# Optimization experiments

Measured on AMD Instinct MI355X. Metric: run time of the kernel, lower is better.

## Reference

```python
import jax, jax.numpy as jnp
import numpy as np

N = 32000      # total nodes (16 graphs x 2000 nodes)
B = 16         # batch of graphs
NPG = N // B   # nodes per graph
K = 1600       # assign_dim (total clusters)
KPG = K // B   # clusters per graph
D = 128        # input_dim == output_feat_dim
E = 512000     # edges (avg degree 16), block-diagonal across graphs


def setup_inputs() -> dict:
    key = jax.random.key(0)
    ks = jax.random.split(key, 12)
    # block-structured edge list: each edge stays within its graph
    epg = E // B
    gid = jnp.repeat(jnp.arange(B, dtype=jnp.int32), epg) * NPG
    src = gid + jax.random.randint(ks[0], (E,), 0, NPG, dtype=jnp.int32)
    dst = gid + jax.random.randint(ks[1], (E,), 0, NPG, dtype=jnp.int32)
    h = jax.random.normal(ks[2], (N, D), dtype=jnp.float32)
    s = 0.05
    return {
        'h': h, 'src': src, 'dst': dst,
        'W1f': jax.random.normal(ks[3], (D, D), jnp.float32) * s,
        'b1f': jnp.zeros((D,), jnp.float32),
        'W2f': jax.random.normal(ks[4], (D, D), jnp.float32) * s,
        'b2f': jnp.zeros((D,), jnp.float32),
        'W1p': jax.random.normal(ks[5], (D, K), jnp.float32) * s,
        'b1p': jnp.zeros((K,), jnp.float32),
        'W2p': jax.random.normal(ks[6], (K, K), jnp.float32) * s,
        'b2p': jnp.zeros((K,), jnp.float32),
    }


def _gin(h, src, dst, W1, b1, W2, b2):
    # mean-aggregate neighbor features, then 2-layer MLP (histocartography GINLayer)
    deg = jax.ops.segment_sum(jnp.ones((src.shape[0],), h.dtype), dst, num_segments=N)
    agg = jax.ops.segment_sum(h[src], dst, num_segments=N)
    agg = agg / jnp.maximum(deg, 1.0)[:, None]
    x = h + agg
    x = jax.nn.relu(x @ W1 + b1)
    x = jax.nn.relu(x @ W2 + b2)
    return x


def _forward(h, src, dst, W1f, b1f, W2f, b2f, W1p, b1p, W2p, b2p):
    feat = _gin(h, src, dst, W1f, b1f, W2f, b2f)            # [N, D]
    assign = _gin(h, src, dst, W1p, b1p, W2p, b2p)          # [N, K]
    # block-diagonal mask: node of graph b can only assign to clusters of graph b
    node_gid = jnp.arange(N, dtype=jnp.int32) // NPG
    col_gid = jnp.arange(K, dtype=jnp.int32) // KPG
    mask = (node_gid[:, None] == col_gid[None, :]).astype(assign.dtype)  # [N, K]
    # masked_softmax(memory_efficient=False): softmax(x*mask)*mask, renormalized
    p = jax.nn.softmax(assign * mask, axis=-1) * mask
    assign = p / (jnp.sum(p, axis=-1, keepdims=True) + 1e-13)
    h_pool = assign.T @ feat                                # [K, D]
    # adj @ assign where adj[dst, src] = 1 (sparse-dense mm via scatter)
    tmp = jax.ops.segment_sum(assign[src], dst, num_segments=N)  # [N, K]
    adj_new = assign.T @ tmp                                # [K, K]
    return adj_new, h_pool


def reference(h, src, dst, W1f, b1f, W2f, b2f, W1p, b1p, W2p, b2p):
    return _forward(h, src, dst, W1f, b1f, W2f, b2f, W1p, b1p, W2p, b2p)
```

## Files before the change

### kernel.cpp

```cpp
#include <hip/hip_runtime.h>

#define N_NODES 32000
#define NPG     2000
#define NGRAPH  16
#define K_ASSIGN 1600
#define KPG     100
#define D_FEAT  128
#define N_EDGES 512000

typedef float f32x4 __attribute__((ext_vector_type(4)));
typedef __bf16 bf16x8 __attribute__((ext_vector_type(8)));

union FragU { unsigned u[4]; bf16x8 v; };

__device__ __forceinline__ float frelu(float v) { return fmaxf(v, 0.0f); }

__device__ __forceinline__ unsigned short f2bf(float f) {
  unsigned u = __float_as_uint(f);
  u += 0x7FFFu + ((u >> 16) & 1u);
  return (unsigned short)(u >> 16);
}
__device__ __forceinline__ float bfLO(unsigned v) { return __uint_as_float(v << 16); }
__device__ __forceinline__ float bfHI(unsigned v) { return __uint_as_float(v & 0xFFFF0000u); }

__global__ __launch_bounds__(256) void edge_hist(
    const int* __restrict__ dst, int* __restrict__ cnt) {
  int e = blockIdx.x * 256 + threadIdx.x;
  if (e < N_EDGES) atomicAdd(&cnt[dst[e]], 1);
}

__global__ __launch_bounds__(256) void scan_counts(
    const int* __restrict__ cnt, int* __restrict__ rowstart) {
  __shared__ int sums[256];
  int t = threadIdx.x;
  int base = t * 125;
  int s = 0;
  for (int i = 0; i < 125; i++) s += cnt[base + i];
  sums[t] = s;
  __syncthreads();
  for (int off = 1; off < 256; off <<= 1) {
    int v = (t >= off) ? sums[t - off] : 0;
    __syncthreads();
    sums[t] += v;
    __syncthreads();
  }
  int run = (t == 0) ? 0 : sums[t - 1];
  for (int i = 0; i < 125; i++) {
    rowstart[base + i] = run;
    run += cnt[base + i];
  }
  if (t == 255) rowstart[32000] = run;
}

__global__ __launch_bounds__(256) void edge_fill(
    const int* __restrict__ src, const int* __restrict__ dst,
    const int* __restrict__ rowstart, int* __restrict__ cursor,
    int* __restrict__ bucket) {
  int e = blockIdx.x * 256 + threadIdx.x;
  if (e < N_EDGES) {
    int d = dst[e];
    int pos = atomicAdd(&cursor[d], 1);
    bucket[rowstart[d] + pos] = src[e];
  }
}

__global__ __launch_bounds__(256) void h_to_bf(
    const float* __restrict__ h, unsigned short* __restrict__ hb) {
  int i = blockIdx.x * 256 + threadIdx.x;
  float4 v = ((const float4*)h)[i];
  ushort4 o;
  o.x = f2bf(v.x); o.y = f2bf(v.y); o.z = f2bf(v.z); o.w = f2bf(v.w);
  ((ushort4*)hb)[i] = o;
}

__global__ __launch_bounds__(256) void gin_gather(
    const int* __restrict__ rowstart, const int* __restrict__ bucket,
    const float* __restrict__ h, const unsigned short* __restrict__ h_bf,
    unsigned short* __restrict__ x_bf) {
  int n = blockIdx.x * 4 + (threadIdx.x >> 6);
  int lane = threadIdx.x & 63;
  int rs = rowstart[n], re = rowstart[n + 1];
  const unsigned* hb = (const unsigned*)h_bf;
  float ax = 0.f, ay = 0.f;
  int e = rs;
  for (; e + 4 <= re; e += 4) {
    unsigned v0 = hb[(size_t)bucket[e] * 64 + lane];
    unsigned v1 = hb[(size_t)bucket[e + 1] * 64 + lane];
    unsigned v2 = hb[(size_t)bucket[e + 2] * 64 + lane];
    unsigned v3 = hb[(size_t)bucket[e + 3] * 64 + lane];
    ax += (bfLO(v0) + bfLO(v1)) + (bfLO(v2) + bfLO(v3));
    ay += (bfHI(v0) + bfHI(v1)) + (bfHI(v2) + bfHI(v3));
  }
  for (; e < re; e++) {
    unsigned v = hb[(size_t)bucket[e] * 64 + lane];
    ax += bfLO(v);
    ay += bfHI(v);
  }
  float invd = 1.0f / fmaxf((float)(re - rs), 1.0f);
  float2 hv = ((const float2*)h)[(size_t)n * 64 + lane];
  unsigned o = ((unsigned)f2bf(hv.y + ay * invd) << 16) | f2bf(hv.x + ax * invd);
  ((unsigned*)x_bf)[(size_t)n * 64 + lane] = o;
}

__global__ __launch_bounds__(256) void transpose_all(
    const float* __restrict__ W1f, const float* __restrict__ W2f,
    const float* __restrict__ W1p, const float* __restrict__ W2p,
    unsigned short* __restrict__ o1, unsigned short* __restrict__ o2,
    unsigned short* __restrict__ o3, unsigned short* __restrict__ o4) {
  __shared__ float tile[32][33];
  int b = blockIdx.x;
  const float* in;
  unsigned short* out;
  int R, C, rb;
  if (b < 16)       { in = W1f; out = o1; R = 128;  C = 128;  rb = b; }
  else if (b < 32)  { in = W2f; out = o2; R = 128;  C = 128;  rb = b - 16; }
  else if (b < 232) { in = W1p; out = o3; R = 128;  C = 1600; rb = b - 32; }
  else              { in = W2p; out = o4; R = 1600; C = 1600; rb = b - 232; }
  int ct = C >> 5;
  int bc = rb % ct, br = rb / ct;
  int r0 = br * 32, c0 = bc * 32;
  int t = threadIdx.x;
#pragma unroll
  for (int i = 0; i < 4; i++) {
    int r = (t >> 5) + i * 8, c = t & 31;
    tile[r][c] = in[(size_t)(r0 + r) * C + c0 + c];
  }
  __syncthreads();
#pragma unroll
  for (int i = 0; i < 4; i++) {
    int c = (t >> 5) + i * 8, r = t & 31;
    out[(size_t)(c0 + c) * R + r0 + r] = f2bf(tile[r][c]);
  }
}

#define FF_STR 136
__global__ __launch_bounds__(512) void feat_fused(
    const unsigned short* __restrict__ x_bf,
    const unsigned short* __restrict__ w1t, const float* __restrict__ b1f,
    const unsigned short* __restrict__ w2t, const float* __restrict__ b2f,
    unsigned short* __restrict__ feat_bf) {
  __shared__ __align__(16) unsigned char smem[2 * 34816];
  unsigned short* xa = (unsigned short*)smem;
  unsigned short* ws = (unsigned short*)(smem + 34816);
  int t = threadIdx.x;
  size_t base = (size_t)blockIdx.x * 128;

#pragma unroll
  for (int i = 0; i < 4; i++) {
    int fi = t + 512 * i;
    int r = fi >> 4, u8 = (fi & 15) * 8;
    *(uint4*)&xa[r * FF_STR + u8] = *(const uint4*)(x_bf + (base + r) * 128 + u8);
    *(uint4*)&ws[r * FF_STR + u8] = *(const uint4*)(w1t + (size_t)r * 128 + u8);
  }
  __syncthreads();

  int w = t >> 6, l = t & 63, lr = l & 15, lg = l >> 4;
  int myrow = 16 * w + lr;
  bf16x8 af[4];
#pragma unroll
  for (int kc = 0; kc < 4; kc++)
    af[kc] = *(bf16x8*)&xa[myrow * FF_STR + 32 * kc + 8 * lg];

  f32x4 p[8];
#pragma unroll
  for (int ntk = 0; ntk < 8; ntk++) {
    p[ntk] = (f32x4){0.f, 0.f, 0.f, 0.f};
    int c = 16 * ntk + lr;
#pragma unroll
    for (int kc = 0; kc < 4; kc++) {
      bf16x8 wf = *(bf16x8*)&ws[c * FF_STR + 32 * kc + 8 * lg];
      p[ntk] = __builtin_amdgcn_mfma_f32_16x16x32_bf16(wf, af[kc], p[ntk], 0, 0, 0);
    }
  }
  __syncthreads();

#pragma unroll
  for (int ntk = 0; ntk < 8; ntk++) {
    int kk0 = 16 * ntk + 4 * lg;
    float4 b1 = *(const float4*)(b1f + kk0);
    ushort4 pk;
    pk.x = f2bf(frelu(p[ntk][0] + b1.x));
    pk.y = f2bf(frelu(p[ntk][1] + b1.y));
    pk.z = f2bf(frelu(p[ntk][2] + b1.z));
    pk.w = f2bf(frelu(p[ntk][3] + b1.w));
    *(ushort4*)&xa[myrow * FF_STR + kk0] = pk;
  }
#pragma unroll
  for (int i = 0; i < 4; i++) {
    int fi = t + 512 * i;
    int r = fi >> 4, u8 = (fi & 15) * 8;
    *(uint4*)&ws[r * FF_STR + u8] = *(const uint4*)(w2t + (size_t)r * 128 + u8);
  }
  __syncthreads();

  bf16x8 a2[4];
#pragma unroll
  for (int kc = 0; kc < 4; kc++)
    a2[kc] = *(bf16x8*)&xa[myrow * FF_STR + 32 * kc + 8 * lg];
#pragma unroll
  for (int nt = 0; nt < 8; nt++) {
    f32x4 q = (f32x4){0.f, 0.f, 0.f, 0.f};
    int c = 16 * nt + lr;
#pragma unroll
    for (int kc = 0; kc < 4; kc++) {
      bf16x8 wf = *(bf16x8*)&ws[c * FF_STR + 32 * kc + 8 * lg];
      q = __builtin_amdgcn_mfma_f32_16x16x32_bf16(wf, a2[kc], q, 0, 0, 0);
    }
    int c0 = 16 * nt + 4 * lg;
    float4 b2 = *(const float4*)(b2f + c0);
    ushort4 pk;
    pk.x = f2bf(frelu(q[0] + b2.x));
    pk.y = f2bf(frelu(q[1] + b2.y));
    pk.z = f2bf(frelu(q[2] + b2.z));
    pk.w = f2bf(frelu(q[3] + b2.w));
    *(ushort4*)&feat_bf[(base + myrow) * 128 + c0] = pk;
  }
}

#define FA_WS 136
#define FA_PS 72
#define FA_W1OFF 17408
#define FA_W2BASE 34816
#define FA_W2OFF 16128
__global__ __launch_bounds__(512) void fused_assign_sm(
    const unsigned short* __restrict__ x_bf, const unsigned short* __restrict__ w1t,
    const float* __restrict__ b1p, const unsigned short* __restrict__ w2t,
    const float* __restrict__ b2p, unsigned short* __restrict__ assign_bf) {
  __shared__ __align__(16) unsigned char smem[67072];
  unsigned short* xt = (unsigned short*)smem;

  int t = threadIdx.x;
  int g = blockIdx.x >> 4;
  int row0 = (blockIdx.x & 15) << 7;
  int n0 = g * NPG + row0;

#pragma unroll
  for (int i = 0; i < 4; i++) {
    int fi = t + 512 * i;
    int r = fi >> 4, u8 = (fi & 15) * 8;
    uint4 v = make_uint4(0, 0, 0, 0);
    if (row0 + r < NPG) v = *(const uint4*)(x_bf + (size_t)(n0 + r) * 128 + u8);
    *(uint4*)&xt[r * FA_WS + u8] = v;
  }
  __syncthreads();

  int w = t >> 6, l = t & 63, lr = l & 15, lg = l >> 4;
  int rh = w >> 1, h = w & 1;

  bf16x8 af[2][4];
#pragma unroll
  for (int ct = 0; ct < 2; ct++)
#pragma unroll
    for (int kc = 0; kc < 4; kc++)
      af[ct][kc] =
          *(bf16x8*)&xt[(32 * rh + 16 * ct + lr) * FA_WS + 32 * kc + 8 * lg];
  __syncthreads();

  {
    unsigned short* w1s = (unsigned short*)smem;
    unsigned short* w2s = (unsigned short*)(smem + FA_W2BASE);
#pragma unroll
    for (int i = 0; i < 2; i++) {
      int fi = t + 512 * i;
      int c = fi >> 4, u8 = (fi & 15) * 8;
      *(uint4*)&w1s[c * FA_WS + u8] = *(const uint4*)(w1t + (size_t)c * 128 + u8);
    }
#pragma unroll
    for (int i = 0; i < 2; i++) {
      int fi = t + 512 * i;
      if (fi < 896) {
        int c = fi >> 3, u8 = (fi & 7) * 8;
        uint4 v = make_uint4(0, 0, 0, 0);
        if (c < KPG)
          v = *(const uint4*)(w2t + (size_t)(g * KPG + c) * K_ASSIGN + u8);
        *(uint4*)&w2s[c * FA_PS + u8] = v;
      }
    }
  }
  __syncthreads();

  f32x4 acc[7][2];
#pragma unroll
  for (int i = 0; i < 7; i++) {
    acc[i][0] = (f32x4){0.f, 0.f, 0.f, 0.f};
    acc[i][1] = (f32x4){0.f, 0.f, 0.f, 0.f};
  }

  for (int cch = 0; cch < 25; cch++) {
    int cur = cch & 1;
    int k0 = cch * 64;
    const unsigned short* w1c = (const unsigned short*)(smem + cur * FA_W1OFF);
    const unsigned short* w2c =
        (const unsigned short*)(smem + FA_W2BASE + cur * FA_W2OFF);
    bool pf = (cch < 24);
    uint4 rA[2], rB[2];
    if (pf) {
      int k1 = k0 + 64;
#pragma unroll
      for (int i = 0; i < 2; i++) {
        int fi = t + 512 * i;
        int c = fi >> 4, u8 = (fi & 15) * 8;
        rA[i] = *(const uint4*)(w1t + (size_t)(k1 + c) * 128 + u8);
      }
#pragma unroll
      for (int i = 0; i < 2; i++) {
        int fi = t + 512 * i;
        rB[i] = make_uint4(0, 0, 0, 0);
        if (fi < 896) {
          int c = fi >> 3, u8 = (fi & 7) * 8;
          if (c < KPG)
            rB[i] = *(const uint4*)(w2t + (size_t)(g * KPG + c) * K_ASSIGN +
                                    k1 + u8);
        }
      }
    }

    f32x4 p[2][2];
#pragma unroll
    for (int nt2 = 0; nt2 < 2; nt2++) {
      p[nt2][0] = (f32x4){0.f, 0.f, 0.f, 0.f};
      p[nt2][1] = (f32x4){0.f, 0.f, 0.f, 0.f};
      int nt = 2 * h + nt2;
#pragma unroll
      for (int kc = 0; kc < 4; kc++) {
        bf16x8 wf = *(bf16x8*)&w1c[(16 * nt + lr) * FA_WS + 32 * kc + 8 * lg];
        p[nt2][0] = __builtin_amdgcn_mfma_f32_16x16x32_bf16(wf, af[0][kc],
                                                            p[nt2][0], 0, 0, 0);
        p[nt2][1] = __builtin_amdgcn_mfma_f32_16x16x32_bf16(wf, af[1][kc],
                                                            p[nt2][1], 0, 0, 0);
      }
    }
    unsigned q[2][2][2];
#pragma unroll
    for (int nt2 = 0; nt2 < 2; nt2++) {
      int kkb = k0 + 16 * (2 * h + nt2) + 4 * lg;
      float4 b1 = *(const float4*)(b1p + kkb);
#pragma unroll
      for (int ct = 0; ct < 2; ct++) {
        float r0 = frelu(p[nt2][ct][0] + b1.x);
        float r1 = frelu(p[nt2][ct][1] + b1.y);
        float r2 = frelu(p[nt2][ct][2] + b1.z);
        float r3 = frelu(p[nt2][ct][3] + b1.w);
        q[nt2][ct][0] = ((unsigned)f2bf(r1) << 16) | f2bf(r0);
        q[nt2][ct][1] = ((unsigned)f2bf(r3) << 16) | f2bf(r2);
      }
    }
    int sA = lr + 32 * (lg & 1);
    int sB = sA + 16;
    bool hi = (lg >= 2);
    FragU pa[2];
#pragma unroll
    for (int ct = 0; ct < 2; ct++) {
      unsigned a0 = (unsigned)__shfl((int)q[0][ct][0], sA, 64);
      unsigned b0 = (unsigned)__shfl((int)q[1][ct][0], sA, 64);
      unsigned a1 = (unsigned)__shfl((int)q[0][ct][1], sA, 64);
      unsigned b1u = (unsigned)__shfl((int)q[1][ct][1], sA, 64);
      unsigned a2 = (unsigned)__shfl((int)q[0][ct][0], sB, 64);
      unsigned b2u = (unsigned)__shfl((int)q[1][ct][0], sB, 64);
      unsigned a3 = (unsigned)__shfl((int)q[0][ct][1], sB, 64);
      unsigned b3u = (unsigned)__shfl((int)q[1][ct][1], sB, 64);
      pa[ct].u[0] = hi ? b0 : a0;
      pa[ct].u[1] = hi ? b1u : a1;
      pa[ct].u[2] = hi ? b2u : a2;
      pa[ct].u[3] = hi ? b3u : a3;
    }
#pragma unroll
    for (int ct2 = 0; ct2 < 7; ct2++) {
      bf16x8 wv = *(bf16x8*)&w2c[(16 * ct2 + lr) * FA_PS + 32 * h + 8 * lg];
      acc[ct2][0] = __builtin_amdgcn_mfma_f32_16x16x32_bf16(wv, pa[0].v,
                                                            acc[ct2][0], 0, 0, 0);
      acc[ct2][1] = __builtin_amdgcn_mfma_f32_16x16x32_bf16(wv, pa[1].v,
                                                            acc[ct2][1], 0, 0, 0);
    }
    if (pf) {
      unsigned short* w1n = (unsigned short*)(smem + (cur ^ 1) * FA_W1OFF);
      unsigned short* w2n =
          (unsigned short*)(smem + FA_W2BASE + (cur ^ 1) * FA_W2OFF);
#pragma unroll
      for (int i = 0; i < 2; i++) {
        int fi = t + 512 * i;
        int c = fi >> 4, u8 = (fi & 15) * 8;
        *(uint4*)&w1n[c * FA_WS + u8] = rA[i];
      }
#pragma unroll
      for (int i = 0; i < 2; i++) {
        int fi = t + 512 * i;
        if (fi < 896) {
          int c = fi >> 3, u8 = (fi & 7) * 8;
          *(uint4*)&w2n[c * FA_PS + u8] = rB[i];
        }
      }
    }
    __syncthreads();
  }

  float* red = (float*)smem;
  if (h == 1) {
#pragma unroll
    for (int ct2 = 0; ct2 < 7; ct2++)
#pragma unroll
      for (int ct = 0; ct < 2; ct++)
        *(f32x4*)&red[((rh * 14 + ct2 * 2 + ct) * 64 + l) * 4] = acc[ct2][ct];
  }
  __syncthreads();
  if (h == 0) {
#pragma unroll
    for (int ct2 = 0; ct2 < 7; ct2++)
#pragma unroll
      for (int ct = 0; ct < 2; ct++)
        acc[ct2][ct] += *(f32x4*)&red[((rh * 14 + ct2 * 2 + ct) * 64 + l) * 4];

#pragma unroll
    for (int ct = 0; ct < 2; ct++) {
      int xrow = row0 + 32 * rh + 16 * ct + lr;
      float v[7][4];
      float m = 0.0f;
#pragma unroll
      for (int ct2 = 0; ct2 < 7; ct2++) {
        int col0 = 16 * ct2 + 4 * lg;
        if (col0 < KPG) {
          float4 b2 = *(const float4*)(b2p + g * KPG + col0);
          v[ct2][0] = frelu(acc[ct2][ct][0] + b2.x);
          v[ct2][1] = frelu(acc[ct2][ct][1] + b2.y);
          v[ct2][2] = frelu(acc[ct2][ct][2] + b2.z);
          v[ct2][3] = frelu(acc[ct2][ct][3] + b2.w);
          m = fmaxf(m, fmaxf(fmaxf(v[ct2][0], v[ct2][1]),
                             fmaxf(v[ct2][2], v[ct2][3])));
        }
      }
      m = fmaxf(m, __shfl_xor(m, 16, 64));
      m = fmaxf(m, __shfl_xor(m, 32, 64));
      float s = 0.0f;
#pragma unroll
      for (int ct2 = 0; ct2 < 7; ct2++) {
        int col0 = 16 * ct2 + 4 * lg;
        if (col0 < KPG) {
          v[ct2][0] = expf(v[ct2][0] - m);
          v[ct2][1] = expf(v[ct2][1] - m);
          v[ct2][2] = expf(v[ct2][2] - m);
          v[ct2][3] = expf(v[ct2][3] - m);
          s += (v[ct2][0] + v[ct2][1]) + (v[ct2][2] + v[ct2][3]);
        }
      }
      s += __shfl_xor(s, 16, 64);
      s += __shfl_xor(s, 32, 64);
      float denom = s + (float)(K_ASSIGN - KPG) * expf(-m);
      float scale = 1.0f / (s + 1e-13f * denom);
      if (xrow < NPG) {
#pragma unroll
        for (int ct2 = 0; ct2 < 7; ct2++) {
          int col0 = 16 * ct2 + 4 * lg;
          if (col0 < KPG) {
            ushort4 pk;
            pk.x = f2bf(v[ct2][0] * scale);
            pk.y = f2bf(v[ct2][1] * scale);
            pk.z = f2bf(v[ct2][2] * scale);
            pk.w = f2bf(v[ct2][3] * scale);
            *(ushort4*)(assign_bf + ((size_t)g * NPG + xrow) * KPG + col0) = pk;
          }
        }
      }
    }
  }
}

__global__ __launch_bounds__(256) void tmp_gather(
    const int* __restrict__ rowstart, const int* __restrict__ bucket,
    const unsigned short* __restrict__ assign_bf, unsigned short* __restrict__ tmp_bf) {
  int n = blockIdx.x * 4 + (threadIdx.x >> 6);
  int lane = threadIdx.x & 63;
  if (lane >= 50) return;
  int rs = rowstart[n], re = rowstart[n + 1];
  const unsigned* ab = (const unsigned*)assign_bf;
  float ax = 0.f, ay = 0.f;
  int e = rs;
  for (; e + 4 <= re; e += 4) {
    unsigned v0 = ab[(size_t)bucket[e] * 50 + lane];
    unsigned v1 = ab[(size_t)bucket[e + 1] * 50 + lane];
    unsigned v2 = ab[(size_t)bucket[e + 2] * 50 + lane];
    unsigned v3 = ab[(size_t)bucket[e + 3] * 50 + lane];
    ax += (bfLO(v0) + bfLO(v1)) + (bfLO(v2) + bfLO(v3));
    ay += (bfHI(v0) + bfHI(v1)) + (bfHI(v2) + bfHI(v3));
  }
  for (; e < re; e++) {
    unsigned v = ab[(size_t)bucket[e] * 50 + lane];
    ax += bfLO(v);
    ay += bfHI(v);
  }
  unsigned o = ((unsigned)f2bf(ay) << 16) | f2bf(ax);
  ((unsigned*)tmp_bf)[(size_t)n * 50 + lane] = o;
}

#define PA_STR 72
#define PA_CH 16
#define PA_CHN 128
__global__ __launch_bounds__(256) void pool_adj_mfma(
    const unsigned short* __restrict__ assign_bf,
    const unsigned short* __restrict__ feat_bf,
    const unsigned short* __restrict__ tmp_bf,
    float* __restrict__ out_adj, float* __restrict__ out_hpool) {
  __shared__ __align__(16) unsigned short as[112 * PA_STR];
  __shared__ __align__(16) unsigned short bs[128 * PA_STR];
  bool is_pool = blockIdx.x < NGRAPH * PA_CH;
  int bb = is_pool ? blockIdx.x : blockIdx.x - NGRAPH * PA_CH;
  int g = bb >> 4, ch = bb & 15;
  int nbase = ch * PA_CHN;
  int lim = NPG - nbase;
  if (lim > PA_CHN) lim = PA_CHN;
  int t = threadIdx.x;
  int w = t >> 6, l = t & 63, lr = l & 15, lg = l >> 4;
  const unsigned* au = (const unsigned*)assign_bf;
  const unsigned* fu = (const unsigned*)feat_bf;
  const unsigned* tu = (const unsigned*)tmp_bf;

  for (int i = t; i < 12 * PA_STR; i += 256) as[100 * PA_STR + i] = 0;
  for (int i = t; i < 28 * PA_STR; i += 256) bs[100 * PA_STR + i] = 0;

  f32x4 acc[7][2];
#pragma unroll
  for (int i = 0; i < 7; i++) {
    acc[i][0] = (f32x4){0.f, 0.f, 0.f, 0.f};
    acc[i][1] = (f32x4){0.f, 0.f, 0.f, 0.f};
  }

  for (int kt = 0; kt < 2; kt++) {
    int nt0 = kt * 64;
    __syncthreads();
#pragma unroll
    for (int i = 0; i < 13; i++) {
      int idx = t + 256 * i;
      if (idx < 3200) {
        int r = idx / 50, cu = idx % 50;
        int nl = nt0 + r;
        unsigned v = 0;
        if (nl < lim) v = au[(size_t)(g * NPG + nbase + nl) * 50 + cu];
        as[(2 * cu) * PA_STR + r] = (unsigned short)(v & 0xFFFFu);
        as[(2 * cu + 1) * PA_STR + r] = (unsigned short)(v >> 16);
      }
    }
    if (is_pool) {
#pragma unroll
      for (int i = 0; i < 16; i++) {
        int idx = t + 256 * i;
        int r = idx >> 6, cu = idx & 63;
        int nl = nt0 + r;
        unsigned v = 0;
        if (nl < lim) v = fu[(size_t)(g * NPG + nbase + nl) * 64 + cu];
        bs[(2 * cu) * PA_STR + r] = (unsigned short)(v & 0xFFFFu);
        bs[(2 * cu + 1) * PA_STR + r] = (unsigned short)(v >> 16);
      }
    } else {
#pragma unroll
      for (int i = 0; i < 13; i++) {
        int idx = t + 256 * i;
        if (idx < 3200) {
          int r = idx / 50, cu = idx % 50;
          int nl = nt0 + r;
          unsigned v = 0;
          if (nl < lim) v = tu[(size_t)(g * NPG + nbase + nl) * 50 + cu];
          bs[(2 * cu) * PA_STR + r] = (unsigned short)(v & 0xFFFFu);
          bs[(2 * cu + 1) * PA_STR + r] = (unsigned short)(v >> 16);
        }
      }
    }
    __syncthreads();
#pragma unroll
    for (int kc = 0; kc < 2; kc++) {
      bf16x8 afr[7];
#pragma unroll
      for (int mt = 0; mt < 7; mt++)
        afr[mt] = *(bf16x8*)&as[(16 * mt + lr) * PA_STR + 32 * kc + 8 * lg];
#pragma unroll
      for (int nt2 = 0; nt2 < 2; nt2++) {
        int nt = 2 * w + nt2;
        bf16x8 bfr = *(bf16x8*)&bs[(16 * nt + lr) * PA_STR + 32 * kc + 8 * lg];
#pragma unroll
        for (int mt = 0; mt < 7; mt++)
          acc[mt][nt2] =
              __builtin_amdgcn_mfma_f32_16x16x32_bf16(afr[mt], bfr, acc[mt][nt2], 0, 0, 0);
      }
    }
  }

  if (is_pool) {
#pragma unroll
    for (int mt = 0; mt < 7; mt++)
#pragma unroll
      for (int nt2 = 0; nt2 < 2; nt2++) {
        int nt = 2 * w + nt2;
#pragma unroll
        for (int r = 0; r < 4; r++) {
          int m = 16 * mt + 4 * lg + r;
          if (m < KPG)
            atomicAdd(out_hpool + ((size_t)g * KPG + m) * 128 + 16 * nt + lr,
                      acc[mt][nt2][r]);
        }
      }
  } else {
#pragma unroll
    for (int mt = 0; mt < 7; mt++)
#pragma unroll
      for (int nt2 = 0; nt2 < 2; nt2++) {
        int nt = 2 * w + nt2;
        if (nt < 7) {
          int k2 = 16 * nt + lr;
          if (k2 < KPG) {
#pragma unroll
            for (int r = 0; r < 4; r++) {
              int m = 16 * mt + 4 * lg + r;
              if (m < KPG)
                atomicAdd(out_adj + ((size_t)g * KPG + m) * K_ASSIGN + g * KPG + k2,
                          acc[mt][nt2][r]);
            }
          }
        }
      }
  }
}

extern "C" void kernel_launch(void* const* d_in, const int* in_sizes, int n_in,
                              void* d_out, int out_size, void* d_ws,
                              size_t ws_size, hipStream_t stream) {
  (void)in_sizes; (void)n_in; (void)ws_size;
  const float* h   = (const float*)d_in[0];
  const int*   src = (const int*)d_in[1];
  const int*   dst = (const int*)d_in[2];
  const float* W1f = (const float*)d_in[3];
  const float* b1f = (const float*)d_in[4];
  const float* W2f = (const float*)d_in[5];
  const float* b2f = (const float*)d_in[6];
  const float* W1p = (const float*)d_in[7];
  const float* b1p = (const float*)d_in[8];
  const float* W2p = (const float*)d_in[9];
  const float* b2p = (const float*)d_in[10];

  float* out_adj   = (float*)d_out;
  float* out_hpool = out_adj + (size_t)K_ASSIGN * K_ASSIGN;

  char* ws = (char*)d_ws;
  int* deg_cnt  = (int*)(ws + 0);
  int* rowstart = (int*)(ws + 128000);
  int* cursor   = (int*)(ws + 256032);
  int* bucket   = (int*)(ws + 384032);
  unsigned short* h_bf      = (unsigned short*)(ws + 2432032);
  unsigned short* x_bf      = (unsigned short*)(ws + 10624032);
  unsigned short* feat_bf   = (unsigned short*)(ws + 18816032);
  unsigned short* assign_bf = (unsigned short*)(ws + 27008032);
  unsigned short* tmp_bf    = (unsigned short*)(ws + 33408032);
  unsigned short* w1f_t     = (unsigned short*)(ws + 39808032);
  unsigned short* w2f_t     = (unsigned short*)(ws + 39840800);
  unsigned short* w1p_t     = (unsigned short*)(ws + 39873568);
  unsigned short* w2p_t     = (unsigned short*)(ws + 40283168);

  hipMemsetAsync(deg_cnt, 0, 128000, stream);
  hipMemsetAsync(cursor, 0, 128000, stream);
  hipMemsetAsync(d_out, 0, (size_t)out_size * sizeof(float), stream);

  edge_hist<<<N_EDGES / 256, 256, 0, stream>>>(dst, deg_cnt);
  scan_counts<<<1, 256, 0, stream>>>(deg_cnt, rowstart);
  edge_fill<<<N_EDGES / 256, 256, 0, stream>>>(src, dst, rowstart, cursor, bucket);

  h_to_bf<<<N_NODES * 128 / 4 / 256, 256, 0, stream>>>(h, h_bf);
  transpose_all<<<16 + 16 + 200 + 2500, 256, 0, stream>>>(
      W1f, W2f, W1p, W2p, w1f_t, w2f_t, w1p_t, w2p_t);

  gin_gather<<<N_NODES / 4, 256, 0, stream>>>(rowstart, bucket, h, h_bf, x_bf);

  feat_fused<<<N_NODES / 128, 512, 0, stream>>>(x_bf, w1f_t, b1f, w2f_t, b2f, feat_bf);

  fused_assign_sm<<<256, 512, 0, stream>>>(x_bf, w1p_t, b1p, w2p_t, b2p, assign_bf);

  tmp_gather<<<N_NODES / 4, 256, 0, stream>>>(rowstart, bucket, assign_bf, tmp_bf);

  pool_adj_mfma<<<NGRAPH * PA_CH * 2, 256, 0, stream>>>(
      assign_bf, feat_bf, tmp_bf, out_adj, out_hpool);
}
```

Measured before the change: 240.7 us.

## Merge prep kernels, swizzle gather block order, and raise MFMA wave priority

Three preprocessing kernels (edge histogram, h to bf16 conversion, weight transposes) are merged into one launch that branches on block index, removing two launch gaps. gin_gather now reads the self term from the bf16 copy of h instead of the fp32 one, cutting read traffic at a small precision cost. Both gather kernels remap block indices so consecutive blocks land on different XCDs, aiming for better L2 locality across the 8 dies. s_setprio is raised around the MFMA sections of the assign kernel so matrix-math waves are scheduled ahead of others.

```diff
diff --git a/kernel.cpp b/kernel.cpp
--- a/kernel.cpp
+++ b/kernel.cpp
@@ -22,12 +22,6 @@
 }
 __device__ __forceinline__ float bfLO(unsigned v) { return __uint_as_float(v << 16); }
 __device__ __forceinline__ float bfHI(unsigned v) { return __uint_as_float(v & 0xFFFF0000u); }
-
-__global__ __launch_bounds__(256) void edge_hist(
-    const int* __restrict__ dst, int* __restrict__ cnt) {
-  int e = blockIdx.x * 256 + threadIdx.x;
-  if (e < N_EDGES) atomicAdd(&cnt[dst[e]], 1);
-}
 
 __global__ __launch_bounds__(256) void scan_counts(
     const int* __restrict__ cnt, int* __restrict__ rowstart) {
@@ -64,20 +58,57 @@
   }
 }
 
-__global__ __launch_bounds__(256) void h_to_bf(
-    const float* __restrict__ h, unsigned short* __restrict__ hb) {
-  int i = blockIdx.x * 256 + threadIdx.x;
-  float4 v = ((const float4*)h)[i];
-  ushort4 o;
-  o.x = f2bf(v.x); o.y = f2bf(v.y); o.z = f2bf(v.z); o.w = f2bf(v.w);
-  ((ushort4*)hb)[i] = o;
+__global__ __launch_bounds__(256) void prep_all(
+    const float* __restrict__ W1f, const float* __restrict__ W2f,
+    const float* __restrict__ W1p, const float* __restrict__ W2p,
+    unsigned short* __restrict__ o1, unsigned short* __restrict__ o2,
+    unsigned short* __restrict__ o3, unsigned short* __restrict__ o4,
+    const float* __restrict__ h, unsigned short* __restrict__ h_bf,
+    const int* __restrict__ dst, int* __restrict__ cnt) {
+  __shared__ float tile[32][33];
+  int b = blockIdx.x;
+  int t = threadIdx.x;
+  if (b >= 6732) {
+    int e = (b - 6732) * 256 + t;
+    if (e < N_EDGES) atomicAdd(&cnt[dst[e]], 1);
+    return;
+  }
+  if (b >= 2732) {
+    int i = (b - 2732) * 256 + t;
+    float4 v = ((const float4*)h)[i];
+    ushort4 o;
+    o.x = f2bf(v.x); o.y = f2bf(v.y); o.z = f2bf(v.z); o.w = f2bf(v.w);
+    ((ushort4*)h_bf)[i] = o;
+    return;
+  }
+  const float* in;
+  unsigned short* out;
+  int R, C, rb;
+  if (b < 16)       { in = W1f; out = o1; R = 128;  C = 128;  rb = b; }
+  else if (b < 32)  { in = W2f; out = o2; R = 128;  C = 128;  rb = b - 16; }
+  else if (b < 232) { in = W1p; out = o3; R = 128;  C = 1600; rb = b - 32; }
+  else              { in = W2p; out = o4; R = 1600; C = 1600; rb = b - 232; }
+  int ct = C >> 5;
+  int bc = rb % ct, br = rb / ct;
+  int r0 = br * 32, c0 = bc * 32;
+#pragma unroll
+  for (int i = 0; i < 4; i++) {
+    int r = (t >> 5) + i * 8, c = t & 31;
+    tile[r][c] = in[(size_t)(r0 + r) * C + c0 + c];
+  }
+  __syncthreads();
+#pragma unroll
+  for (int i = 0; i < 4; i++) {
+    int c = (t >> 5) + i * 8, r = t & 31;
+    out[(size_t)(c0 + c) * R + r0 + r] = f2bf(tile[r][c]);
+  }
 }
 
 __global__ __launch_bounds__(256) void gin_gather(
     const int* __restrict__ rowstart, const int* __restrict__ bucket,
-    const float* __restrict__ h, const unsigned short* __restrict__ h_bf,
-    unsigned short* __restrict__ x_bf) {
-  int n = blockIdx.x * 4 + (threadIdx.x >> 6);
+    const unsigned short* __restrict__ h_bf, unsigned short* __restrict__ x_bf) {
+  int bid = (int)(blockIdx.x & 7) * 1000 + (int)(blockIdx.x >> 3);
+  int n = bid * 4 + (threadIdx.x >> 6);
   int lane = threadIdx.x & 63;
   int rs = rowstart[n], re = rowstart[n + 1];
   const unsigned* hb = (const unsigned*)h_bf;
@@ -97,40 +128,10 @@
     ay += bfHI(v);
   }
   float invd = 1.0f / fmaxf((float)(re - rs), 1.0f);
-  float2 hv = ((const float2*)h)[(size_t)n * 64 + lane];
-  unsigned o = ((unsigned)f2bf(hv.y + ay * invd) << 16) | f2bf(hv.x + ax * invd);
+  unsigned hv = hb[(size_t)n * 64 + lane];
+  unsigned o = ((unsigned)f2bf(bfHI(hv) + ay * invd) << 16) |
+               f2bf(bfLO(hv) + ax * invd);
   ((unsigned*)x_bf)[(size_t)n * 64 + lane] = o;
-}
-
-__global__ __launch_bounds__(256) void transpose_all(
-    const float* __restrict__ W1f, const float* __restrict__ W2f,
-    const float* __restrict__ W1p, const float* __restrict__ W2p,
-    unsigned short* __restrict__ o1, unsigned short* __restrict__ o2,
-    unsigned short* __restrict__ o3, unsigned short* __restrict__ o4) {
-  __shared__ float tile[32][33];
-  int b = blockIdx.x;
-  const float* in;
-  unsigned short* out;
-  int R, C, rb;
-  if (b < 16)       { in = W1f; out = o1; R = 128;  C = 128;  rb = b; }
-  else if (b < 32)  { in = W2f; out = o2; R = 128;  C = 128;  rb = b - 16; }
-  else if (b < 232) { in = W1p; out = o3; R = 128;  C = 1600; rb = b - 32; }
-  else              { in = W2p; out = o4; R = 1600; C = 1600; rb = b - 232; }
-  int ct = C >> 5;
-  int bc = rb % ct, br = rb / ct;
-  int r0 = br * 32, c0 = bc * 32;
-  int t = threadIdx.x;
-#pragma unroll
-  for (int i = 0; i < 4; i++) {
-    int r = (t >> 5) + i * 8, c = t & 31;
-    tile[r][c] = in[(size_t)(r0 + r) * C + c0 + c];
-  }
-  __syncthreads();
-#pragma unroll
-  for (int i = 0; i < 4; i++) {
-    int c = (t >> 5) + i * 8, r = t & 31;
-    out[(size_t)(c0 + c) * R + r0 + r] = f2bf(tile[r][c]);
-  }
 }
 
 #define FF_STR 136
@@ -316,6 +317,7 @@
     }
 
     f32x4 p[2][2];
+    __builtin_amdgcn_s_setprio(1);
 #pragma unroll
     for (int nt2 = 0; nt2 < 2; nt2++) {
       p[nt2][0] = (f32x4){0.f, 0.f, 0.f, 0.f};
@@ -330,6 +332,7 @@
                                                             p[nt2][1], 0, 0, 0);
       }
     }
+    __builtin_amdgcn_s_setprio(0);
     unsigned q[2][2][2];
 #pragma unroll
     for (int nt2 = 0; nt2 < 2; nt2++) {
@@ -364,6 +367,7 @@
       pa[ct].u[2] = hi ? b2u : a2;
       pa[ct].u[3] = hi ? b3u : a3;
     }
+    __builtin_amdgcn_s_setprio(1);
 #pragma unroll
     for (int ct2 = 0; ct2 < 7; ct2++) {
       bf16x8 wv = *(bf16x8*)&w2c[(16 * ct2 + lr) * FA_PS + 32 * h + 8 * lg];
@@ -372,6 +376,7 @@
       acc[ct2][1] = __builtin_amdgcn_mfma_f32_16x16x32_bf16(wv, pa[1].v,
                                                             acc[ct2][1], 0, 0, 0);
     }
+    __builtin_amdgcn_s_setprio(0);
     if (pf) {
       unsigned short* w1n = (unsigned short*)(smem + (cur ^ 1) * FA_W1OFF);
       unsigned short* w2n =
@@ -467,7 +472,8 @@
 __global__ __launch_bounds__(256) void tmp_gather(
     const int* __restrict__ rowstart, const int* __restrict__ bucket,
     const unsigned short* __restrict__ assign_bf, unsigned short* __restrict__ tmp_bf) {
-  int n = blockIdx.x * 4 + (threadIdx.x >> 6);
+  int bid = (int)(blockIdx.x & 7) * 1000 + (int)(blockIdx.x >> 3);
+  int n = bid * 4 + (threadIdx.x >> 6);
   int lane = threadIdx.x & 63;
   if (lane >= 50) return;
   int rs = rowstart[n], re = rowstart[n + 1];
@@ -656,15 +662,13 @@
   hipMemsetAsync(cursor, 0, 128000, stream);
   hipMemsetAsync(d_out, 0, (size_t)out_size * sizeof(float), stream);
 
-  edge_hist<<<N_EDGES / 256, 256, 0, stream>>>(dst, deg_cnt);
+  prep_all<<<8732, 256, 0, stream>>>(W1f, W2f, W1p, W2p, w1f_t, w2f_t, w1p_t,
+                                     w2p_t, h, h_bf, dst, deg_cnt);
+
   scan_counts<<<1, 256, 0, stream>>>(deg_cnt, rowstart);
   edge_fill<<<N_EDGES / 256, 256, 0, stream>>>(src, dst, rowstart, cursor, bucket);
 
-  h_to_bf<<<N_NODES * 128 / 4 / 256, 256, 0, stream>>>(h, h_bf);
-  transpose_all<<<16 + 16 + 200 + 2500, 256, 0, stream>>>(
-      W1f, W2f, W1p, W2p, w1f_t, w2f_t, w1p_t, w2p_t);
-
-  gin_gather<<<N_NODES / 4, 256, 0, stream>>>(rowstart, bucket, h, h_bf, x_bf);
+  gin_gather<<<N_NODES / 4, 256, 0, stream>>>(rowstart, bucket, h_bf, x_bf);
 
   feat_fused<<<N_NODES / 128, 512, 0, stream>>>(x_bf, w1f_t, b1f, w2f_t, b2f, feat_bf);
 
```

Measured after the change: 228.3 us. -5.2%, faster.
